# Optimization experiments

Hardware: AMD Instinct MI355X
Metric: run time of the kernel (lower is better)

Reference implementation:

```python
import jax, jax.numpy as jnp
import numpy as np
from jax import lax

EPS = 1e-5
NEG_SLOPE = 0.01

def setup_inputs() -> dict:
    key = jax.random.key(0)
    ks = jax.random.split(key, 9)
    B, Cin, Cout, D, H, W = 2, 32, 64, 20, 20, 20
    x = jax.random.normal(ks[0], (B, Cin, D, H, W), dtype=jnp.float32)
    conv_w = jax.random.normal(ks[1], (Cout, Cin, 3, 3, 3), dtype=jnp.float32) * 0.05
    conv_b = jnp.zeros((Cout,), dtype=jnp.float32)
    gamma = jnp.ones((Cout,), dtype=jnp.float32)
    beta = jnp.zeros((Cout,), dtype=jnp.float32)
    wq = jax.random.normal(ks[2], (Cout, Cout), dtype=jnp.float32) * 0.05
    bq = jnp.zeros((Cout,), dtype=jnp.float32)
    wk = jax.random.normal(ks[3], (Cout, Cout), dtype=jnp.float32) * 0.05
    bk = jnp.zeros((Cout,), dtype=jnp.float32)
    wv = jax.random.normal(ks[4], (Cout, Cout), dtype=jnp.float32) * 0.05
    bv = jnp.zeros((Cout,), dtype=jnp.float32)
    return {"x": x, "conv_w": conv_w, "conv_b": conv_b, "gamma": gamma,
            "beta": beta, "wq": wq, "bq": bq, "wk": wk, "bk": bk,
            "wv": wv, "bv": bv}

def reference(x, conv_w, conv_b, gamma, beta, wq, bq, wk, bk, wv, bv):
    # Conv3d k=3, stride=1, padding=1 (SAME)
    y = lax.conv_general_dilated(
        x, conv_w, window_strides=(1, 1, 1), padding='SAME',
        dimension_numbers=('NCDHW', 'OIDHW', 'NCDHW'))
    y = y + conv_b[None, :, None, None, None]
    # InstanceNorm3d: normalize over spatial dims per (batch, channel)
    mu = jnp.mean(y, axis=(2, 3, 4), keepdims=True)
    var = jnp.mean(jnp.square(y - mu), axis=(2, 3, 4), keepdims=True)
    y = (y - mu) * lax.rsqrt(var + EPS)
    y = y * gamma[None, :, None, None, None] + beta[None, :, None, None, None]
    # LeakyReLU
    y = jnp.where(y >= 0, y, NEG_SLOPE * y)
    # Attention: 1x1x1 convs -> flatten -> bmm softmax bmm (no scaling)
    B, C, D, H, W = y.shape
    N = D * H * W
    f = y.reshape(B, C, N)                                  # [B, C, N]
    q = jnp.einsum('oc,bcn->bon', wq, f) + bq[None, :, None]
    k = jnp.einsum('oc,bcn->bon', wk, f) + bk[None, :, None]
    v = jnp.einsum('oc,bcn->bon', wv, f) + bv[None, :, None]
    att = jax.nn.softmax(jnp.einsum('bcn,bcm->bnm', q, k), axis=-1)  # [B,N,N]
    out = jnp.einsum('bck,bqk->bcq', v, att)                # [B, C, N]
    return out.reshape(B, C, D, H, W)
```

## Files before the change

### kernel.cpp

```cpp
#include <hip/hip_runtime.h>
#include <math.h>

#define CIN   32
#define COUT  64
#define DD    20
#define PD    22
#define PSP   (PD*PD*PD)
#define NSP   8000
#define BB    2
#define EPSN  1e-5f
#define SLOPE 0.01f
#define LOG2E 1.4426950408889634f

#define NT     250
#define SPLITS 8
#define QUADS  63

#define COG 4
#define OG  8

typedef float  f32x16 __attribute__((ext_vector_type(16)));
typedef short  short8 __attribute__((ext_vector_type(8)));

__device__ __forceinline__ unsigned short f2bf_rne(float x) {
    unsigned u = __float_as_uint(x);
    unsigned r = (u + 0x7FFFu + ((u >> 16) & 1u)) >> 16;
    return (unsigned short)r;
}
__device__ __forceinline__ float bf2f(unsigned short h) {
    return __uint_as_float(((unsigned)h) << 16);
}
__device__ __forceinline__ short8 ld_frag(const unsigned short* p) {
    uint4 t = *reinterpret_cast<const uint4*>(p);
    return __builtin_bit_cast(short8, t);
}
__device__ __forceinline__ void gload_lds16(const void* gsrc, void* ldst) {
    typedef __attribute__((address_space(1))) const unsigned int GU;
    typedef __attribute__((address_space(3))) unsigned int LU;
    __builtin_amdgcn_global_load_lds((GU*)gsrc, (LU*)ldst, 16, 0, 0);
}
__device__ __forceinline__ float exp2_fast(float x) {
    float r;
    asm("v_exp_f32 %0, %1" : "=v"(r) : "v"(x));
    return r;
}
__device__ __forceinline__ float wsum(float x) {
    #pragma unroll
    for (int off = 1; off < 64; off <<= 1) x += __shfl_xor(x, off, 64);
    return x;
}

__global__ void pad_k(const float* __restrict__ x, float* __restrict__ xp) {
    int idx = blockIdx.x * blockDim.x + threadIdx.x;
    if (idx >= BB * CIN * PSP) return;
    int pw = idx % PD;
    int ph = (idx / PD) % PD;
    int pd = (idx / (PD * PD)) % PD;
    int bc = idx / PSP;
    float v = 0.f;
    if (pw >= 1 && pw <= DD && ph >= 1 && ph <= DD && pd >= 1 && pd <= DD)
        v = x[(size_t)bc * NSP + ((size_t)(pd - 1) * DD + (ph - 1)) * DD + (pw - 1)];
    xp[idx] = v;
}

__global__ __launch_bounds__(256) void conv3d_k(const float* __restrict__ xp,
                                                const float* __restrict__ w,
                                                const float* __restrict__ bias,
                                                float* __restrict__ y,
                                                float2* __restrict__ part) {
    int blk = blockIdx.x;
    int vb  = blk & 31;
    int cg  = (blk >> 5) & 15;
    int b   = blk >> 9;
    int vox = vb * 256 + threadIdx.x;
    bool valid = vox < NSP;
    int v  = valid ? vox : 0;
    int w_ = v % DD;
    int h_ = (v / DD) % DD;
    int d_ = v / (DD * DD);
    int pvox = ((d_ + 1) * PD + (h_ + 1)) * PD + (w_ + 1);
    const float* xb = xp + (size_t)b * CIN * PSP + pvox;

    float acc[COG];
    #pragma unroll
    for (int j = 0; j < COG; ++j) acc[j] = 0.f;

    for (int ci = 0; ci < CIN; ++ci) {
        const float* xc = xb + (size_t)ci * PSP;
        float xv[27];
        #pragma unroll
        for (int kd = 0; kd < 3; ++kd)
            #pragma unroll
            for (int kh = 0; kh < 3; ++kh)
                #pragma unroll
                for (int kw = 0; kw < 3; ++kw)
                    xv[(kd * 3 + kh) * 3 + kw] =
                        xc[(kd - 1) * (PD * PD) + (kh - 1) * PD + (kw - 1)];
        #pragma unroll
        for (int j = 0; j < COG; ++j) {
            int co = cg * COG + j;
            const float* wr = w + ((size_t)co * CIN + ci) * 27;
            float a = acc[j];
            #pragma unroll
            for (int t = 0; t < 27; ++t) a += xv[t] * wr[t];
            acc[j] = a;
        }
    }

    __shared__ float2 wred[4][COG];
    int wv = threadIdx.x >> 6;
    int ln = threadIdx.x & 63;
    #pragma unroll
    for (int j = 0; j < COG; ++j) {
        int co = cg * COG + j;
        float val = valid ? acc[j] + bias[co] : 0.f;
        if (valid) y[((size_t)b * COUT + co) * NSP + vox] = val;
        float s  = wsum(val);
        float ss = wsum(val * val);
        if (ln == 0) wred[wv][j] = make_float2(s, ss);
    }
    __syncthreads();
    if (threadIdx.x < COG) {
        int j = threadIdx.x;
        float s = 0.f, ss = 0.f;
        #pragma unroll
        for (int w2 = 0; w2 < 4; ++w2) { s += wred[w2][j].x; ss += wred[w2][j].y; }
        part[((size_t)(b * COUT + cg * COG + j)) * 32 + vb] = make_float2(s, ss);
    }
}

__global__ __launch_bounds__(256) void qkv_k(const float* __restrict__ yraw,
                      const float2* __restrict__ part,
                      const float* __restrict__ gamma, const float* __restrict__ beta,
                      const float* __restrict__ wq, const float* __restrict__ bq,
                      const float* __restrict__ wk, const float* __restrict__ bk,
                      const float* __restrict__ wv, const float* __restrict__ bv,
                      unsigned short* __restrict__ Qfh,
                      unsigned short* __restrict__ Kfh,
                      unsigned short* __restrict__ Vf) {
    int blk = blockIdx.x;
    int vb  = blk & 31;
    int og  = (blk >> 5) & 7;
    int b   = blk >> 8;
    int n   = vb * 256 + threadIdx.x;
    bool valid = n < NSP;
    int nn  = valid ? n : 0;
    const float* fb = yraw + (size_t)b * COUT * NSP + nn;

    __shared__ float smean[COUT], srstd[COUT];
    if (threadIdx.x < COUT) {
        int c = threadIdx.x;
        float s = 0.f, ss = 0.f;
        #pragma unroll 8
        for (int ch = 0; ch < 32; ++ch) {
            float2 p = part[(size_t)(b * COUT + c) * 32 + ch];
            s += p.x; ss += p.y;
        }
        float mean = s * (1.f / NSP);
        smean[c] = mean;
        srstd[c] = rsqrtf(ss * (1.f / NSP) - mean * mean + EPSN);
    }
    __syncthreads();

    float aq[OG], ak[OG], av[OG];
    #pragma unroll
    for (int j = 0; j < OG; ++j) {
        int o = og * OG + j;
        aq[j] = bq[o]; ak[j] = bk[o]; av[j] = bv[o];
    }
    for (int c = 0; c < COUT; ++c) {
        float fc = (fb[(size_t)c * NSP] - smean[c]) * srstd[c] * gamma[c] + beta[c];
        fc = fc >= 0.f ? fc : SLOPE * fc;
        #pragma unroll
        for (int j = 0; j < OG; ++j) {
            int o = og * OG + j;
            aq[j] += wq[o * COUT + c] * fc;
            ak[j] += wk[o * COUT + c] * fc;
            av[j] += wv[o * COUT + c] * fc;
        }
    }
    if (!valid) return;

    int t  = n >> 5;
    int kk = n & 31;
    unsigned short qh[OG], kh[OG];
    #pragma unroll
    for (int j = 0; j < OG; ++j) {
        qh[j] = f2bf_rne(aq[j] * LOG2E);
        kh[j] = f2bf_rne(ak[j]);
    }
    size_t qko = ((size_t)((b * NT + t) * 4 + (og >> 1)) * 2 + (og & 1)) * 256 + kk * 8;
    *reinterpret_cast<uint4*>(Qfh + qko) = *reinterpret_cast<const uint4*>(qh);
    *reinterpret_cast<uint4*>(Kfh + qko) = *reinterpret_cast<const uint4*>(kh);
    {
        int Y = kk >> 4, hf = (kk >> 3) & 1, e = kk & 7;
        size_t vbase = ((size_t)((b * NT + t) * 2 + Y) * 2 + (og >> 2)) * 512
                     + hf * 256 + e;
        #pragma unroll
        for (int j = 0; j < OG; ++j)
            Vf[vbase + ((og & 3) * 8 + j) * 8] = f2bf_rne(av[j]);
    }
}

__global__ __launch_bounds__(256, 4) void attn_pass1_mfma(
        const unsigned short* __restrict__ Qfh,
        const unsigned short* __restrict__ Kfh,
        const unsigned short* __restrict__ Vf,
        float* __restrict__ pm, float* __restrict__ pl, float* __restrict__ pacc) {
    int bid   = blockIdx.x;
    int split = bid / (BB * QUADS);
    int rem   = bid % (BB * QUADS);
    int b     = rem / QUADS;
    int quad  = rem % QUADS;
    int wave  = threadIdx.x >> 6;
    int lane  = threadIdx.x & 63;
    int col   = lane & 31;
    int half  = lane >> 5;
    int qt    = quad * 4 + wave;
    bool qvalid = qt < NT;
    int qtc   = qvalid ? qt : NT - 1;
    int bNT   = b * NT;

    int tstart = (split * NT) / SPLITS;
    int tend   = ((split + 1) * NT) / SPLITS;
    int nkt    = tend - tstart;
    int npair  = nkt >> 1;
    int odd    = nkt & 1;

    __shared__ __align__(16) char ldsbuf[2][16384];

    short8 qfh[4];
    {
        const unsigned short* qp = Qfh + (size_t)(bNT + qtc) * 2048 + lane * 8;
        #pragma unroll
        for (int c = 0; c < 4; ++c) qfh[c] = ld_frag(qp + c * 512);
    }

    int wo = wave * 1024;
    int go = wo + lane * 16;

    auto STAGET = [&](int bufi, int slot, int tg) {
        size_t tb = (size_t)(bNT + tg) * 2048;
        char* l = &ldsbuf[bufi][slot * 8192];
        gload_lds16((const char*)(Kfh + tb) + go, l + wo);
        gload_lds16((const char*)(Vf  + tb) + go, l + 4096 + wo);
    };

    f32x16 oacc0 = {};
    f32x16 oacc1 = {};
    float m = -3e38f, lsum = 0.f;

    auto SM_PV = [&](const f32x16& s, const unsigned short* lv) {
        float a0 = fmaxf(fmaxf(s[0],  s[1]),  s[2]);
        float a1 = fmaxf(fmaxf(s[3],  s[4]),  s[5]);
        float a2 = fmaxf(fmaxf(s[6],  s[7]),  s[8]);
        float a3 = fmaxf(fmaxf(s[9],  s[10]), s[11]);
        float a4 = fmaxf(fmaxf(s[12], s[13]), s[14]);
        float tmax = fmaxf(fmaxf(fmaxf(a0, a1), a2), fmaxf(fmaxf(a3, a4), s[15]));
        tmax = fmaxf(tmax, __shfl_xor(tmax, 32, 64));
        if (__any(tmax > m + 11.5f)) {
            float newm  = fmaxf(m, tmax);
            float scale = exp2_fast(m - newm);
            lsum *= scale;
            #pragma unroll
            for (int r = 0; r < 16; ++r) { oacc0[r] *= scale; oacc1[r] *= scale; }
            m = newm;
        }
        short8 pf0, pf1;
        float ls;
        {
            float p[8];
            #pragma unroll
            for (int r = 0; r < 8; ++r) p[r] = exp2_fast(s[r] - m);
            ls = ((p[0] + p[1]) + (p[2] + p[3])) + ((p[4] + p[5]) + (p[6] + p[7]));
            unsigned W[4], X[4];
            #pragma unroll
            for (int j = 0; j < 4; ++j)
                asm("v_cvt_pk_bf16_f32 %0, %1, %2" : "=v"(W[j]) : "v"(p[2 * j]), "v"(p[2 * j + 1]));
            #pragma unroll
            for (int j = 0; j < 4; ++j) X[j] = (unsigned)__shfl_xor((int)W[j], 32, 64);
            uint4 u = half ? make_uint4(X[2], X[3], W[2], W[3])
                           : make_uint4(W[0], W[1], X[0], X[1]);
            pf0 = __builtin_bit_cast(short8, u);
        }
        {
            float p[8];
            #pragma unroll
            for (int r = 0; r < 8; ++r) p[r] = exp2_fast(s[r + 8] - m);
            ls += ((p[0] + p[1]) + (p[2] + p[3])) + ((p[4] + p[5]) + (p[6] + p[7]));
            unsigned W[4], X[4];
            #pragma unroll
            for (int j = 0; j < 4; ++j)
                asm("v_cvt_pk_bf16_f32 %0, %1, %2" : "=v"(W[j]) : "v"(p[2 * j]), "v"(p[2 * j + 1]));
            #pragma unroll
            for (int j = 0; j < 4; ++j) X[j] = (unsigned)__shfl_xor((int)W[j], 32, 64);
            uint4 u = half ? make_uint4(X[2], X[3], W[2], W[3])
                           : make_uint4(W[0], W[1], X[0], X[1]);
            pf1 = __builtin_bit_cast(short8, u);
        }
        lsum += ls;
        short8 v00 = ld_frag(lv + 0 * 512 + lane * 8);
        short8 v10 = ld_frag(lv + 1 * 512 + lane * 8);
        __builtin_amdgcn_s_setprio(1);
        oacc0 = __builtin_amdgcn_mfma_f32_32x32x16_bf16(v00, pf0, oacc0, 0, 0, 0);
        oacc1 = __builtin_amdgcn_mfma_f32_32x32x16_bf16(v10, pf0, oacc1, 0, 0, 0);
        __builtin_amdgcn_s_setprio(0);
        short8 v01 = ld_frag(lv + 2 * 512 + lane * 8);
        short8 v11 = ld_frag(lv + 3 * 512 + lane * 8);
        __builtin_amdgcn_s_setprio(1);
        oacc0 = __builtin_amdgcn_mfma_f32_32x32x16_bf16(v01, pf1, oacc0, 0, 0, 0);
        oacc1 = __builtin_amdgcn_mfma_f32_32x32x16_bf16(v11, pf1, oacc1, 0, 0, 0);
        __builtin_amdgcn_s_setprio(0);
    };

    STAGET(0, 0, tstart);
    STAGET(0, 1, tstart + 1);

    for (int p = 0; p < npair; ++p) {
        __syncthreads();
        int nb = (p + 1) & 1;
        if (p + 1 < npair) {
            STAGET(nb, 0, tstart + 2 * p + 2);
            STAGET(nb, 1, tstart + 2 * p + 3);
        } else if (odd) {
            STAGET(nb, 0, tstart + 2 * p + 2);
        }
        const unsigned short* base = (const unsigned short*)&ldsbuf[p & 1][0];
        const unsigned short* lk0 = base;
        const unsigned short* lv0 = base + 2048;
        const unsigned short* lk1 = base + 4096;
        const unsigned short* lv1 = base + 6144;

        f32x16 s0 = {}, s1 = {};
        __builtin_amdgcn_s_setprio(1);
        #pragma unroll
        for (int c = 0; c < 4; ++c) {
            short8 k0 = ld_frag(lk0 + c * 512 + lane * 8);
            s0 = __builtin_amdgcn_mfma_f32_32x32x16_bf16(k0, qfh[c], s0, 0, 0, 0);
        }
        #pragma unroll
        for (int c = 0; c < 4; ++c) {
            short8 k1 = ld_frag(lk1 + c * 512 + lane * 8);
            s1 = __builtin_amdgcn_mfma_f32_32x32x16_bf16(k1, qfh[c], s1, 0, 0, 0);
        }
        __builtin_amdgcn_s_setprio(0);

        SM_PV(s0, lv0);
        SM_PV(s1, lv1);
    }
    if (odd) {
        __syncthreads();
        const unsigned short* base = (const unsigned short*)&ldsbuf[npair & 1][0];
        f32x16 s0 = {};
        __builtin_amdgcn_s_setprio(1);
        #pragma unroll
        for (int c = 0; c < 4; ++c) {
            short8 k0 = ld_frag(base + c * 512 + lane * 8);
            s0 = __builtin_amdgcn_mfma_f32_32x32x16_bf16(k0, qfh[c], s0, 0, 0, 0);
        }
        __builtin_amdgcn_s_setprio(0);
        SM_PV(s0, base + 2048);
    }

    if (!qvalid) return;
    int q0 = qt * 32;
    float lfull = lsum + __shfl_xor(lsum, 32, 64);
    size_t base = (size_t)b * SPLITS + split;
    if (lane < 32) {
        pm[base * NSP + q0 + col] = m;
        pl[base * NSP + q0 + col] = lfull;
    }
    float* pa = pacc + base * (size_t)(COUT * NSP) + q0 + col;
    #pragma unroll
    for (int r = 0; r < 16; ++r) {
        int crow = (r & 3) + 8 * (r >> 2) + 4 * half;
        pa[(size_t)crow * NSP]        = oacc0[r];
        pa[(size_t)(crow + 32) * NSP] = oacc1[r];
    }
}

__global__ void attn_combine_k(const float* __restrict__ pm, const float* __restrict__ pl,
                               const float* __restrict__ pacc, float* __restrict__ out) {
    int idx = blockIdx.x * blockDim.x + threadIdx.x;
    const int N4 = NSP / 4;
    if (idx >= BB * COUT * N4) return;
    int n4 = idx % N4;
    int c  = (idx / N4) % COUT;
    int b  = idx / (N4 * COUT);
    int n  = n4 * 4;

    float4 M = make_float4(-1e30f, -1e30f, -1e30f, -1e30f);
    #pragma unroll
    for (int j = 0; j < SPLITS; ++j) {
        float4 v = *reinterpret_cast<const float4*>(&pm[((size_t)b * SPLITS + j) * NSP + n]);
        M.x = fmaxf(M.x, v.x); M.y = fmaxf(M.y, v.y);
        M.z = fmaxf(M.z, v.z); M.w = fmaxf(M.w, v.w);
    }
    float4 L = make_float4(0.f, 0.f, 0.f, 0.f);
    float4 O = make_float4(0.f, 0.f, 0.f, 0.f);
    #pragma unroll
    for (int j = 0; j < SPLITS; ++j) {
        size_t base = (size_t)b * SPLITS + j;
        float4 pmv = *reinterpret_cast<const float4*>(&pm[base * NSP + n]);
        float4 plv = *reinterpret_cast<const float4*>(&pl[base * NSP + n]);
        float4 pav = *reinterpret_cast<const float4*>(&pacc[(base * COUT + c) * NSP + n]);
        float4 wgt;
        wgt.x = exp2_fast(pmv.x - M.x); wgt.y = exp2_fast(pmv.y - M.y);
        wgt.z = exp2_fast(pmv.z - M.z); wgt.w = exp2_fast(pmv.w - M.w);
        L.x += plv.x * wgt.x; L.y += plv.y * wgt.y;
        L.z += plv.z * wgt.z; L.w += plv.w * wgt.w;
        O.x += pav.x * wgt.x; O.y += pav.y * wgt.y;
        O.z += pav.z * wgt.z; O.w += pav.w * wgt.w;
    }
    float4 r;
    r.x = O.x / L.x; r.y = O.y / L.y; r.z = O.z / L.z; r.w = O.w / L.w;
    *reinterpret_cast<float4*>(&out[((size_t)(b * COUT + c)) * NSP + n]) = r;
}

extern "C" void kernel_launch(void* const* d_in, const int* in_sizes, int n_in,
                              void* d_out, int out_size, void* d_ws, size_t ws_size,
                              hipStream_t stream) {
    const float* x      = (const float*)d_in[0];
    const float* conv_w = (const float*)d_in[1];
    const float* conv_b = (const float*)d_in[2];
    const float* gamma  = (const float*)d_in[3];
    const float* beta   = (const float*)d_in[4];
    const float* wq     = (const float*)d_in[5];
    const float* bq     = (const float*)d_in[6];
    const float* wk     = (const float*)d_in[7];
    const float* bk     = (const float*)d_in[8];
    const float* wv     = (const float*)d_in[9];
    const float* bv     = (const float*)d_in[10];
    float* out = (float*)d_out;

    const int ELEMS = BB * COUT * NSP;
    char* w8 = (char*)d_ws;
    float*  y    = (float*)w8;
    float2* part = (float2*)(w8 + 4096000);
    unsigned short* Qfh = (unsigned short*)(w8 + 4128768);
    unsigned short* Kfh = Qfh + (size_t)ELEMS;
    unsigned short* Vf  = Kfh + (size_t)ELEMS;
    float* pm   = (float*)(Vf + (size_t)ELEMS);
    float* pl   = pm + (size_t)BB * SPLITS * NSP;
    float* pacc = pl + (size_t)BB * SPLITS * NSP;
    float* xpad = pacc;

    pad_k<<<(BB * CIN * PSP + 255) / 256, 256, 0, stream>>>(x, xpad);
    conv3d_k<<<BB * 16 * 32, 256, 0, stream>>>(xpad, conv_w, conv_b, y, part);
    qkv_k<<<BB * 8 * 32, 256, 0, stream>>>(y, part, gamma, beta,
                                           wq, bq, wk, bk, wv, bv,
                                           Qfh, Kfh, Vf);
    attn_pass1_mfma<<<SPLITS * BB * QUADS, 256, 0, stream>>>(Qfh, Kfh, Vf,
                                                             pm, pl, pacc);
    attn_combine_k<<<(BB * COUT * (NSP / 4) + 255) / 256, 256, 0, stream>>>(pm, pl, pacc, out);
}
```

Baseline: 133.1 us.

## Merge softmax max update across tile pairs, split QKV output groups, unroll conv

The attention loop now computes one running-max update over both 32-key tiles in a pair before the exponentials, where it previously did a separate max/rescale per tile. This halves the cross-lane shuffles and rescale branches. The QKV projection kernel halves its output-channel group (8 to 4) and doubles its grid, changing Q/K/V store offsets to match. The conv input-channel loop also gets a partial unroll. More QKV blocks raise parallelism but reread the normalized activations more often.

```diff
diff --git a/kernel.cpp b/kernel.cpp
--- a/kernel.cpp
+++ b/kernel.cpp
@@ -17,7 +17,7 @@
 #define QUADS  63
 
 #define COG 4
-#define OG  8
+#define OG  4
 
 typedef float  f32x16 __attribute__((ext_vector_type(16)));
 typedef short  short8 __attribute__((ext_vector_type(8)));
@@ -85,6 +85,7 @@
     #pragma unroll
     for (int j = 0; j < COG; ++j) acc[j] = 0.f;
 
+    #pragma unroll 2
     for (int ci = 0; ci < CIN; ++ci) {
         const float* xc = xb + (size_t)ci * PSP;
         float xv[27];
@@ -140,8 +141,8 @@
                       unsigned short* __restrict__ Vf) {
     int blk = blockIdx.x;
     int vb  = blk & 31;
-    int og  = (blk >> 5) & 7;
-    int b   = blk >> 8;
+    int og  = (blk >> 5) & 15;
+    int b   = blk >> 9;
     int n   = vb * 256 + threadIdx.x;
     bool valid = n < NSP;
     int nn  = valid ? n : 0;
@@ -189,16 +190,17 @@
         qh[j] = f2bf_rne(aq[j] * LOG2E);
         kh[j] = f2bf_rne(ak[j]);
     }
-    size_t qko = ((size_t)((b * NT + t) * 4 + (og >> 1)) * 2 + (og & 1)) * 256 + kk * 8;
-    *reinterpret_cast<uint4*>(Qfh + qko) = *reinterpret_cast<const uint4*>(qh);
-    *reinterpret_cast<uint4*>(Kfh + qko) = *reinterpret_cast<const uint4*>(kh);
+    size_t qko = ((size_t)((b * NT + t) * 4 + (og >> 2)) * 2 + ((og >> 1) & 1)) * 256
+               + kk * 8 + (og & 1) * 4;
+    *reinterpret_cast<uint2*>(Qfh + qko) = *reinterpret_cast<const uint2*>(qh);
+    *reinterpret_cast<uint2*>(Kfh + qko) = *reinterpret_cast<const uint2*>(kh);
     {
         int Y = kk >> 4, hf = (kk >> 3) & 1, e = kk & 7;
-        size_t vbase = ((size_t)((b * NT + t) * 2 + Y) * 2 + (og >> 2)) * 512
+        size_t vbase = ((size_t)((b * NT + t) * 2 + Y) * 2 + (og >> 3)) * 512
                      + hf * 256 + e;
         #pragma unroll
         for (int j = 0; j < OG; ++j)
-            Vf[vbase + ((og & 3) * 8 + j) * 8] = f2bf_rne(av[j]);
+            Vf[vbase + ((og & 7) * 4 + j) * 8] = f2bf_rne(av[j]);
     }
 }
 
@@ -250,22 +252,19 @@
     f32x16 oacc1 = {};
     float m = -3e38f, lsum = 0.f;
 
-    auto SM_PV = [&](const f32x16& s, const unsigned short* lv) {
-        float a0 = fmaxf(fmaxf(s[0],  s[1]),  s[2]);
-        float a1 = fmaxf(fmaxf(s[3],  s[4]),  s[5]);
-        float a2 = fmaxf(fmaxf(s[6],  s[7]),  s[8]);
-        float a3 = fmaxf(fmaxf(s[9],  s[10]), s[11]);
-        float a4 = fmaxf(fmaxf(s[12], s[13]), s[14]);
-        float tmax = fmaxf(fmaxf(fmaxf(a0, a1), a2), fmaxf(fmaxf(a3, a4), s[15]));
-        tmax = fmaxf(tmax, __shfl_xor(tmax, 32, 64));
-        if (__any(tmax > m + 11.5f)) {
-            float newm  = fmaxf(m, tmax);
-            float scale = exp2_fast(m - newm);
-            lsum *= scale;
-            #pragma unroll
-            for (int r = 0; r < 16; ++r) { oacc0[r] *= scale; oacc1[r] *= scale; }
-            m = newm;
-        }
+    auto BUILD_PF = [&](const float* p) -> short8 {
+        unsigned W[4], X[4];
+        #pragma unroll
+        for (int j = 0; j < 4; ++j)
+            asm("v_cvt_pk_bf16_f32 %0, %1, %2" : "=v"(W[j]) : "v"(p[2 * j]), "v"(p[2 * j + 1]));
+        #pragma unroll
+        for (int j = 0; j < 4; ++j) X[j] = (unsigned)__shfl_xor((int)W[j], 32, 64);
+        uint4 u = half ? make_uint4(X[2], X[3], W[2], W[3])
+                       : make_uint4(W[0], W[1], X[0], X[1]);
+        return __builtin_bit_cast(short8, u);
+    };
+
+    auto EXP_PV = [&](const f32x16& s, const unsigned short* lv) {
         short8 pf0, pf1;
         float ls;
         {
@@ -273,30 +272,14 @@
             #pragma unroll
             for (int r = 0; r < 8; ++r) p[r] = exp2_fast(s[r] - m);
             ls = ((p[0] + p[1]) + (p[2] + p[3])) + ((p[4] + p[5]) + (p[6] + p[7]));
-            unsigned W[4], X[4];
-            #pragma unroll
-            for (int j = 0; j < 4; ++j)
-                asm("v_cvt_pk_bf16_f32 %0, %1, %2" : "=v"(W[j]) : "v"(p[2 * j]), "v"(p[2 * j + 1]));
-            #pragma unroll
-            for (int j = 0; j < 4; ++j) X[j] = (unsigned)__shfl_xor((int)W[j], 32, 64);
-            uint4 u = half ? make_uint4(X[2], X[3], W[2], W[3])
-                           : make_uint4(W[0], W[1], X[0], X[1]);
-            pf0 = __builtin_bit_cast(short8, u);
+            pf0 = BUILD_PF(p);
         }
         {
             float p[8];
             #pragma unroll
             for (int r = 0; r < 8; ++r) p[r] = exp2_fast(s[r + 8] - m);
             ls += ((p[0] + p[1]) + (p[2] + p[3])) + ((p[4] + p[5]) + (p[6] + p[7]));
-            unsigned W[4], X[4];
-            #pragma unroll
-            for (int j = 0; j < 4; ++j)
-                asm("v_cvt_pk_bf16_f32 %0, %1, %2" : "=v"(W[j]) : "v"(p[2 * j]), "v"(p[2 * j + 1]));
-            #pragma unroll
-            for (int j = 0; j < 4; ++j) X[j] = (unsigned)__shfl_xor((int)W[j], 32, 64);
-            uint4 u = half ? make_uint4(X[2], X[3], W[2], W[3])
-                           : make_uint4(W[0], W[1], X[0], X[1]);
-            pf1 = __builtin_bit_cast(short8, u);
+            pf1 = BUILD_PF(p);
         }
         lsum += ls;
         short8 v00 = ld_frag(lv + 0 * 512 + lane * 8);
@@ -313,6 +296,44 @@
         __builtin_amdgcn_s_setprio(0);
     };
 
+    auto MAXUPD2 = [&](const f32x16& s0, const f32x16& s1) {
+        float mx[8];
+        #pragma unroll
+        for (int r = 0; r < 8; ++r)
+            mx[r] = fmaxf(fmaxf(s0[r], s0[r + 8]), fmaxf(s1[r], s1[r + 8]));
+        float a0 = fmaxf(fmaxf(mx[0], mx[1]), mx[2]);
+        float a1 = fmaxf(fmaxf(mx[3], mx[4]), mx[5]);
+        float a2 = fmaxf(fmaxf(mx[6], mx[7]), a0);
+        float tmax = fmaxf(a1, a2);
+        tmax = fmaxf(tmax, __shfl_xor(tmax, 32, 64));
+        if (__any(tmax > m + 11.5f)) {
+            float newm  = fmaxf(m, tmax);
+            float scale = exp2_fast(m - newm);
+            lsum *= scale;
+            #pragma unroll
+            for (int r = 0; r < 16; ++r) { oacc0[r] *= scale; oacc1[r] *= scale; }
+            m = newm;
+        }
+    };
+    auto MAXUPD1 = [&](const f32x16& s) {
+        float mx[8];
+        #pragma unroll
+        for (int r = 0; r < 8; ++r) mx[r] = fmaxf(s[r], s[r + 8]);
+        float a0 = fmaxf(fmaxf(mx[0], mx[1]), mx[2]);
+        float a1 = fmaxf(fmaxf(mx[3], mx[4]), mx[5]);
+        float a2 = fmaxf(fmaxf(mx[6], mx[7]), a0);
+        float tmax = fmaxf(a1, a2);
+        tmax = fmaxf(tmax, __shfl_xor(tmax, 32, 64));
+        if (__any(tmax > m + 11.5f)) {
+            float newm  = fmaxf(m, tmax);
+            float scale = exp2_fast(m - newm);
+            lsum *= scale;
+            #pragma unroll
+            for (int r = 0; r < 16; ++r) { oacc0[r] *= scale; oacc1[r] *= scale; }
+            m = newm;
+        }
+    };
+
     STAGET(0, 0, tstart);
     STAGET(0, 1, tstart + 1);
 
@@ -345,8 +366,9 @@
         }
         __builtin_amdgcn_s_setprio(0);
 
-        SM_PV(s0, lv0);
-        SM_PV(s1, lv1);
+        MAXUPD2(s0, s1);
+        EXP_PV(s0, lv0);
+        EXP_PV(s1, lv1);
     }
     if (odd) {
         __syncthreads();
@@ -359,7 +381,8 @@
             s0 = __builtin_amdgcn_mfma_f32_32x32x16_bf16(k0, qfh[c], s0, 0, 0, 0);
         }
         __builtin_amdgcn_s_setprio(0);
-        SM_PV(s0, base + 2048);
+        MAXUPD1(s0);
+        EXP_PV(s0, base + 2048);
     }
 
     if (!qvalid) return;
@@ -447,9 +470,9 @@
 
     pad_k<<<(BB * CIN * PSP + 255) / 256, 256, 0, stream>>>(x, xpad);
     conv3d_k<<<BB * 16 * 32, 256, 0, stream>>>(xpad, conv_w, conv_b, y, part);
-    qkv_k<<<BB * 8 * 32, 256, 0, stream>>>(y, part, gamma, beta,
-                                           wq, bq, wk, bk, wv, bv,
-                                           Qfh, Kfh, Vf);
+    qkv_k<<<BB * 16 * 32, 256, 0, stream>>>(y, part, gamma, beta,
+                                            wq, bq, wk, bk, wv, bv,
+                                            Qfh, Kfh, Vf);
     attn_pass1_mfma<<<SPLITS * BB * QUADS, 256, 0, stream>>>(Qfh, Kfh, Vf,
                                                              pm, pl, pacc);
     attn_combine_k<<<(BB * COUT * (NSP / 4) + 255) / 256, 256, 0, stream>>>(pm, pl, pacc, out);
```

Measured after the change: 138.6 us. +4.1%, slower.
